# Optimization experiments

Hardware: AMD Instinct MI355X
Metric: run time of the kernel (lower is better)

The kernel has to match this reference:

```python
import jax, jax.numpy as jnp
import numpy as np

DIM = 1024
NUM_HEADS = 16
DIM_HEAD = 64
INNER = NUM_HEADS * DIM_HEAD  # 1024
SCALE = DIM_HEAD ** -0.5


def setup_inputs() -> dict:
    key = jax.random.key(0)
    ks = jax.random.split(key, 8)
    B, SQ, SK = 2, 2048, 4096
    x = jax.random.normal(ks[0], (B, SQ, DIM), dtype=jnp.float32)
    context = jax.random.normal(ks[1], (B, SK, DIM), dtype=jnp.float32)
    # LayerNorm params
    ln_gamma = jnp.ones((DIM,), jnp.float32)
    ln_beta = jnp.zeros((DIM,), jnp.float32)
    # Linear weights, stored as [in, out] so y = x @ W (torch Linear weight transposed)
    w_q = jax.random.normal(ks[2], (DIM, INNER), dtype=jnp.float32) / np.sqrt(DIM)
    w_kv = jax.random.normal(ks[3], (DIM, 2 * INNER), dtype=jnp.float32) / np.sqrt(DIM)
    w_out = jax.random.normal(ks[4], (INNER, DIM), dtype=jnp.float32) / np.sqrt(INNER)
    b_out = jnp.zeros((DIM,), jnp.float32)
    # torch init is 0.0 (tanh(0)=0); use a nonzero value so output/grads are nontrivial
    gate = jnp.array([0.5], jnp.float32)
    return {"x": x, "context": context, "ln_gamma": ln_gamma, "ln_beta": ln_beta,
            "w_q": w_q, "w_kv": w_kv, "w_out": w_out, "b_out": b_out, "gate": gate}


def _layernorm(x, gamma, beta, eps=1e-5):
    mu = jnp.mean(x, axis=-1, keepdims=True)
    var = jnp.mean(jnp.square(x - mu), axis=-1, keepdims=True)
    return (x - mu) * jax.lax.rsqrt(var + eps) * gamma + beta


def reference(x, context, ln_gamma, ln_beta, w_q, w_kv, w_out, b_out, gate):
    B, SQ, _ = x.shape
    SK = context.shape[1]
    xn = _layernorm(x, ln_gamma, ln_beta)
    q = (xn @ w_q).reshape(B, SQ, NUM_HEADS, DIM_HEAD)
    kv = context @ w_kv
    k, v = jnp.split(kv, 2, axis=-1)
    k = k.reshape(B, SK, NUM_HEADS, DIM_HEAD)
    v = v.reshape(B, SK, NUM_HEADS, DIM_HEAD)
    # scores: [B, H, SQ, SK]
    scores = jnp.einsum('bqhd,bkhd->bhqk', q * SCALE, k)
    attn = jax.nn.softmax(scores, axis=-1)
    out = jnp.einsum('bhqk,bkhd->bqhd', attn, v).reshape(B, SQ, INNER)
    out = out @ w_out + b_out
    return out * jnp.tanh(gate[0])
```

## Files before the change

### kernel.cpp

```cpp
#include <hip/hip_runtime.h>
#include <hip/hip_bf16.h>
#include <stdint.h>

#define DIMM  1024
#define NHEAD 16
#define DHEAD 64
#define BB    2
#define SQL   2048
#define SKL   4096
#define KVW   2048
#define NT    (SKL / 64)

typedef __attribute__((ext_vector_type(8))) short short8;
typedef __attribute__((ext_vector_type(4))) float f32x4;
typedef __attribute__((ext_vector_type(16))) float f32x16;
typedef __attribute__((ext_vector_type(4))) unsigned short us4;

typedef const __attribute__((address_space(1))) uint32_t gu32_t;
typedef __attribute__((address_space(3))) uint32_t lu32_t;

#define GLDS16(gp, lp) __builtin_amdgcn_global_load_lds((gu32_t*)(gp), (lu32_t*)(lp), 16, 0, 0)

static __device__ __forceinline__ unsigned short f2bf(float f) {
  union { float f; uint32_t u; } v; v.f = f;
  uint32_t r = v.u + 0x7fffu + ((v.u >> 16) & 1u);
  return (unsigned short)(r >> 16);
}

__global__ __launch_bounds__(256) void k_prep(const float* __restrict__ wq,
                                              const float* __restrict__ wkv,
                                              const float* __restrict__ wot,
                                              const float* __restrict__ x,
                                              const float* __restrict__ gamma,
                                              const float* __restrict__ beta,
                                              const float* __restrict__ ctx,
                                              unsigned short* __restrict__ WQT,
                                              unsigned short* __restrict__ WKVT,
                                              unsigned short* __restrict__ WOT,
                                              unsigned short* __restrict__ XN,
                                              unsigned short* __restrict__ CTXB) {
  const int bid = blockIdx.x;
  const int tid = threadIdx.x;

  if (bid < 4096) {
    __shared__ float tile[32][33];
    const float* in; unsigned short* out; int N, bx, by;
    if (bid < 1024)      {                    in = wq;  out = WQT;  N = 1024; bx = bid & 31; by = bid >> 5; }
    else if (bid < 3072) { int l = bid - 1024; in = wkv; out = WKVT; N = 2048; bx = l & 63; by = l >> 6; }
    else                 { int l = bid - 3072; in = wot; out = WOT;  N = 1024; bx = l & 31; by = l >> 5; }
    const int K = 1024;
    const int n0 = bx * 32, k0 = by * 32;
    const int tx = tid & 31, ty = tid >> 5;
    #pragma unroll
    for (int i = 0; i < 4; i++)
      tile[ty + i * 8][tx] = in[(size_t)(k0 + ty + i * 8) * N + n0 + tx];
    __syncthreads();
    #pragma unroll
    for (int i = 0; i < 4; i++)
      out[(size_t)(n0 + ty + i * 8) * K + k0 + tx] = f2bf(tile[tx][ty + i * 8]);
  } else if (bid < 8192) {
    const int row = bid - 4096;
    const float* xr = x + (size_t)row * DIMM;
    float4 v = *(const float4*)(xr + tid * 4);
    float s = v.x + v.y + v.z + v.w;
    float ss = v.x * v.x + v.y * v.y + v.z * v.z + v.w * v.w;
    #pragma unroll
    for (int m = 1; m < 64; m <<= 1) {
      s += __shfl_xor(s, m);
      ss += __shfl_xor(ss, m);
    }
    __shared__ float red[8];
    const int wid = tid >> 6, lane = tid & 63;
    if (lane == 0) { red[wid] = s; red[4 + wid] = ss; }
    __syncthreads();
    s = red[0] + red[1] + red[2] + red[3];
    ss = red[4] + red[5] + red[6] + red[7];
    float mu = s * (1.0f / DIMM);
    float var = ss * (1.0f / DIMM) - mu * mu;
    float rstd = rsqrtf(var + 1e-5f);
    float4 g = *(const float4*)(gamma + tid * 4);
    float4 bt = *(const float4*)(beta + tid * 4);
    us4 o;
    o.x = f2bf((v.x - mu) * rstd * g.x + bt.x);
    o.y = f2bf((v.y - mu) * rstd * g.y + bt.y);
    o.z = f2bf((v.z - mu) * rstd * g.z + bt.z);
    o.w = f2bf((v.w - mu) * rstd * g.w + bt.w);
    *(us4*)(XN + (size_t)row * DIMM + tid * 4) = o;
  } else {
    size_t i = ((size_t)(bid - 8192) * 256 + tid) * 8;
    float4 v0 = *(const float4*)(ctx + i);
    float4 v1 = *(const float4*)(ctx + i + 4);
    union { us4 h[2]; short8 s; } o;
    o.h[0].x = f2bf(v0.x); o.h[0].y = f2bf(v0.y); o.h[0].z = f2bf(v0.z); o.h[0].w = f2bf(v0.w);
    o.h[1].x = f2bf(v1.x); o.h[1].y = f2bf(v1.y); o.h[1].z = f2bf(v1.z); o.h[1].w = f2bf(v1.w);
    *(short8*)(CTXB + i) = o.s;
  }
}

__global__ __launch_bounds__(256) void k_proj(const unsigned short* __restrict__ CTXB,
                                              const unsigned short* __restrict__ XN,
                                              const unsigned short* __restrict__ WKVT,
                                              const unsigned short* __restrict__ WQT,
                                              unsigned short* __restrict__ KVB,
                                              unsigned short* __restrict__ QB) {
  __shared__ unsigned short lA[2][128 * 32];
  __shared__ unsigned short lB[2][128 * 32];
  const int tid = threadIdx.x;
  const int wid = tid >> 6, lane = tid & 63;
  const int kg = lane >> 4, lr = lane & 15;
  const int wr = wid >> 1, wc = wid & 1;
  const int K = 1024, nt = 32;

  const int bid = blockIdx.x;
  const int xcd = bid & 7;
  const int idx = bid >> 3;
  const bool isQ = (idx >= 128);
  int im, in_, N;
  const unsigned short* Ap;
  const unsigned short* Bw;
  unsigned short* Cout;
  if (isQ) { int q = idx - 128; im = xcd * 4 + (q & 3);   in_ = q >> 2;   Bw = WQT;  Cout = QB;  N = 1024; Ap = XN; }
  else     {                    im = xcd * 8 + (idx & 7); in_ = idx >> 3; Bw = WKVT; Cout = KVB; N = 2048; Ap = CTXB; }
  const size_t baseB = (size_t)in_ * 128 * K;
  const unsigned short* Abf = Ap + (size_t)im * 128 * K;

  int ed[2], grow[2], gcol[2];
  #pragma unroll
  for (int j = 0; j < 2; j++) {
    int e = wid * 1024 + j * 512 + lane * 8;
    ed[j] = e;
    int row = e >> 5;
    grow[j] = row;
    gcol[j] = (((e >> 3) & 3) ^ ((row >> 1) & 3)) << 3;
  }

  f32x4 acc[4][4];
  #pragma unroll
  for (int m = 0; m < 4; m++)
    #pragma unroll
    for (int n = 0; n < 4; n++) {
      f32x4 z = {0.0f, 0.0f, 0.0f, 0.0f};
      acc[m][n] = z;
    }

  auto STAGE = [&](int bufi, int t) {
    int k0 = t << 5;
    #pragma unroll
    for (int j = 0; j < 2; j++) {
      GLDS16(Abf + (size_t)grow[j] * K + k0 + gcol[j], &lA[bufi][ed[j]]);
      GLDS16(Bw + baseB + (size_t)grow[j] * K + k0 + gcol[j], &lB[bufi][ed[j]]);
    }
  };
  auto COMPUTE = [&](int bufi) {
    short8 a[4], b[4];
    #pragma unroll
    for (int m = 0; m < 4; m++) {
      int row = wr * 64 + m * 16 + lr;
      a[m] = *(const short8*)&lA[bufi][row * 32 + ((kg ^ ((row >> 1) & 3)) << 3)];
    }
    #pragma unroll
    for (int n = 0; n < 4; n++) {
      int row = wc * 64 + n * 16 + lr;
      b[n] = *(const short8*)&lB[bufi][row * 32 + ((kg ^ ((row >> 1) & 3)) << 3)];
    }
    #pragma unroll
    for (int m = 0; m < 4; m++)
      #pragma unroll
      for (int n = 0; n < 4; n++)
        acc[m][n] = __builtin_amdgcn_mfma_f32_16x16x32_bf16(a[m], b[n], acc[m][n], 0, 0, 0);
  };

  STAGE(0, 0);
  __syncthreads();
  int buf = 0;
  for (int t = 0; t < nt; t++) {
    if (t + 1 < nt) STAGE(buf ^ 1, t + 1);
    COMPUTE(buf);
    __syncthreads();
    buf ^= 1;
  }

  const int r0 = im * 128 + wr * 64;
  const int c0 = in_ * 128 + wc * 64;
  #pragma unroll
  for (int m = 0; m < 4; m++)
    #pragma unroll
    for (int n = 0; n < 4; n++)
      #pragma unroll
      for (int j = 0; j < 4; j++)
        Cout[(size_t)(r0 + m * 16 + kg * 4 + j) * N + c0 + n * 16 + lr] = f2bf(acc[m][n][j]);
}

__global__ __launch_bounds__(256) void k_out(const unsigned short* __restrict__ A,
                                             const unsigned short* __restrict__ BT,
                                             float* __restrict__ C,
                                             const float* __restrict__ bias,
                                             const float* __restrict__ gate) {
  __shared__ unsigned short lA[2][64 * 32];
  __shared__ unsigned short lB[2][128 * 32];
  const int tid = threadIdx.x;
  const int wid = tid >> 6, lane = tid & 63;
  const int kg = lane >> 4, lr = lane & 15;
  const int wr = wid >> 1, wc = wid & 1;
  const int K = 1024, nt = 32, N = 1024;

  const int bid = blockIdx.x;
  const int xcd = bid & 7;
  const int idx = bid >> 3;
  const int im = xcd * 8 + (idx & 7);
  const int in_ = idx >> 3;
  const size_t baseA = (size_t)im * 64 * K;
  const size_t baseB = (size_t)in_ * 128 * K;

  int eA, arow, acol;
  {
    int e = tid * 8;
    eA = e;
    int row = e >> 5;
    arow = row; acol = (((e >> 3) & 3) ^ ((row >> 1) & 3)) << 3;
  }
  int eB[2], brow[2], bcol[2];
  #pragma unroll
  for (int j = 0; j < 2; j++) {
    int e = tid * 8 + j * 2048;
    eB[j] = e;
    int row = e >> 5;
    brow[j] = row; bcol[j] = (((e >> 3) & 3) ^ ((row >> 1) & 3)) << 3;
  }

  f32x4 acc[2][4];
  #pragma unroll
  for (int m = 0; m < 2; m++)
    #pragma unroll
    for (int n = 0; n < 4; n++) {
      f32x4 z = {0.0f, 0.0f, 0.0f, 0.0f};
      acc[m][n] = z;
    }

  auto STAGE = [&](int bufi, int t) {
    int k0 = t << 5;
    GLDS16(A + baseA + (size_t)arow * K + k0 + acol, &lA[bufi][eA]);
    #pragma unroll
    for (int j = 0; j < 2; j++)
      GLDS16(BT + baseB + (size_t)brow[j] * K + k0 + bcol[j], &lB[bufi][eB[j]]);
  };

  STAGE(0, 0);
  __syncthreads();
  int buf = 0;
  for (int t = 0; t < nt; t++) {
    if (t + 1 < nt) STAGE(buf ^ 1, t + 1);
    short8 a[2], b[4];
    #pragma unroll
    for (int m = 0; m < 2; m++) {
      int row = wr * 32 + m * 16 + lr;
      a[m] = *(const short8*)&lA[buf][row * 32 + ((kg ^ ((row >> 1) & 3)) << 3)];
    }
    #pragma unroll
    for (int n = 0; n < 4; n++) {
      int row = wc * 64 + n * 16 + lr;
      b[n] = *(const short8*)&lB[buf][row * 32 + ((kg ^ ((row >> 1) & 3)) << 3)];
    }
    #pragma unroll
    for (int m = 0; m < 2; m++)
      #pragma unroll
      for (int n = 0; n < 4; n++)
        acc[m][n] = __builtin_amdgcn_mfma_f32_16x16x32_bf16(a[m], b[n], acc[m][n], 0, 0, 0);
    __syncthreads();
    buf ^= 1;
  }

  const int r0 = im * 64 + wr * 32;
  const int c0 = in_ * 128 + wc * 64;
  float gl = tanhf(gate[0]);
  #pragma unroll
  for (int m = 0; m < 2; m++)
    #pragma unroll
    for (int n = 0; n < 4; n++)
      #pragma unroll
      for (int j = 0; j < 4; j++) {
        int col = c0 + n * 16 + lr;
        C[(size_t)(r0 + m * 16 + kg * 4 + j) * N + col] = (acc[m][n][j] + bias[col]) * gl;
      }
}

__global__ __launch_bounds__(256, 4) void k_attn(const unsigned short* __restrict__ Q,
                                                 const unsigned short* __restrict__ KV,
                                                 unsigned short* __restrict__ O) {
  __shared__ unsigned short sK[2][64 * 64];
  __shared__ unsigned short sV[2][64 * 64];

  const int tid = threadIdx.x;
  const int wave = tid >> 6, lane = tid & 63;
  const int wq = wave & 1, wk = wave >> 1;
  const int l31 = lane & 31, hi = lane >> 5;

  const int wid_b = blockIdx.x;
  const int work = (wid_b & 7) * 128 + (wid_b >> 3);
  const int qb = work & 31, bh = work >> 5;
  const int b = bh >> 4, h = bh & 15;

  const unsigned short* Qp = Q + (size_t)b * SQL * DIMM + h * DHEAD;
  const unsigned short* Kp = KV + (size_t)b * SKL * KVW + h * DHEAD;
  const unsigned short* Vp = Kp + DIMM;

  const int qr0 = qb * 64 + wq * 32;

  const unsigned short* ksrc[2]; int kdst[2];
  const unsigned short* vsrc[2]; int vdst[2];
  #pragma unroll
  for (int j = 0; j < 2; j++) {
    int e = (tid + j * 256) * 8;
    int row = e >> 6;
    int col = (((e >> 3) & 7) ^ (row & 7)) << 3;
    ksrc[j] = Kp + (size_t)row * KVW + col;
    kdst[j] = e;
    int g = tid + j * 256;
    int key = (g >> 5) * 4 + ((g >> 1) & 3);
    int d0v = ((g >> 3) & 3) * 16 + (g & 1) * 8;
    vsrc[j] = Vp + (size_t)key * KVW + d0v;
    vdst[j] = g * 8;
  }

  auto STAGE = [&](int bufi, int kt) {
    size_t off = (size_t)kt * 64 * KVW;
    #pragma unroll
    for (int j = 0; j < 2; j++) GLDS16(ksrc[j] + off, &sK[bufi][kdst[j]]);
    #pragma unroll
    for (int j = 0; j < 2; j++) GLDS16(vsrc[j] + off, &sV[bufi][vdst[j]]);
  };

  short8 qa[4];
  #pragma unroll
  for (int t = 0; t < 4; t++) {
    short8 v = *(const short8*)(Qp + (size_t)(qr0 + l31) * DIMM + t * 16 + hi * 8);
    #pragma unroll
    for (int j = 0; j < 8; j++) {
      union { float f; uint32_t u; } c;
      c.u = ((uint32_t)(unsigned short)v[j]) << 16;
      v[j] = (short)f2bf(c.f * 0.1803368801111f);
    }
    qa[t] = v;
  }

  f32x16 oacc[2];
  #pragma unroll
  for (int d2 = 0; d2 < 2; d2++)
    #pragma unroll
    for (int r = 0; r < 16; r++) oacc[d2][r] = 0.0f;
  float rs = 0.0f;

  const uint32_t sVb0 = (uint32_t)(size_t)(lu32_t*)&sV[0][0] +
                        (uint32_t)(hi * 1024 + ((lane >> 4) & 1) * 128 + (lane & 15) * 8);

  STAGE(0, 0);
  __syncthreads();

  union u4s8 { uint32_t u[4]; short8 s; };

  int buf = 0;
  for (int kt = 0; kt < NT; kt++) {
    if (kt + 1 < NT) STAGE(buf ^ 1, kt + 1);

    short8 kbf[4];
    {
      int row = wk * 32 + l31;
      #pragma unroll
      for (int t = 0; t < 4; t++) {
        int gl = t * 2 + hi;
        kbf[t] = *(const short8*)&sK[buf][row * 64 + ((gl ^ (row & 7)) << 3)];
      }
    }

    f32x16 sc;
    #pragma unroll
    for (int r = 0; r < 16; r++) sc[r] = 0.0f;
    #pragma unroll
    for (int t = 0; t < 4; t++)
      sc = __builtin_amdgcn_mfma_f32_32x32x16_bf16(kbf[t], qa[t], sc, 0, 0, 0);

    float p[16];
    #pragma unroll
    for (int r = 0; r < 16; r++) {
      p[r] = __builtin_amdgcn_exp2f(sc[r]);
      rs += p[r];
    }
    uint32_t w[8];
    #pragma unroll
    for (int i = 0; i < 8; i++)
      asm("v_cvt_pk_bf16_f32 %0, %1, %2" : "=v"(w[i]) : "v"(p[2 * i]), "v"(p[2 * i + 1]));
    asm("v_permlane32_swap_b32 %0, %1" : "+v"(w[0]), "+v"(w[2]));
    asm("v_permlane32_swap_b32 %0, %1" : "+v"(w[1]), "+v"(w[3]));
    asm("v_permlane32_swap_b32 %0, %1" : "+v"(w[4]), "+v"(w[6]));
    asm("v_permlane32_swap_b32 %0, %1" : "+v"(w[5]), "+v"(w[7]));
    u4s8 paf[2];
    paf[0].u[0] = w[0]; paf[0].u[1] = w[1]; paf[0].u[2] = w[2]; paf[0].u[3] = w[3];
    paf[1].u[0] = w[4]; paf[1].u[1] = w[5]; paf[1].u[2] = w[6]; paf[1].u[3] = w[7];

    u4s8 vb[2][2];
    {
      uint32_t tb = sVb0 + (uint32_t)(buf * 8192 + wk * 4096);
      #pragma unroll
      for (int d2 = 0; d2 < 2; d2++)
        #pragma unroll
        for (int ks = 0; ks < 2; ks++) {
          uint2 t0, t1;
          uint32_t a0 = tb + (uint32_t)(ks * 2048 + d2 * 256);
          asm volatile("ds_read_b64_tr_b16 %0, %1" : "=v"(t0) : "v"(a0));
          asm volatile("ds_read_b64_tr_b16 %0, %1" : "=v"(t1) : "v"(a0 + 512u));
          vb[d2][ks].u[0] = t0.x; vb[d2][ks].u[1] = t0.y;
          vb[d2][ks].u[2] = t1.x; vb[d2][ks].u[3] = t1.y;
        }
    }
    asm volatile("s_waitcnt lgkmcnt(0)" ::: "memory");
    __builtin_amdgcn_sched_barrier(0);

    #pragma unroll
    for (int d2 = 0; d2 < 2; d2++)
      #pragma unroll
      for (int ks = 0; ks < 2; ks++)
        oacc[d2] = __builtin_amdgcn_mfma_f32_32x32x16_bf16(paf[ks].s, vb[d2][ks].s, oacc[d2], 0, 0, 0);

    __syncthreads();
    buf ^= 1;
  }

  float* sRed = (float*)&sK[0][0];
  float* sRs  = (float*)&sV[0][0];
  if (wk == 1) {
    #pragma unroll
    for (int d2 = 0; d2 < 2; d2++)
      #pragma unroll
      for (int r = 0; r < 16; r++)
        sRed[((wq * 2 + d2) * 16 + r) * 64 + lane] = oacc[d2][r];
    sRs[wq * 64 + lane] = rs;
  }
  __syncthreads();
  if (wk == 0) {
    #pragma unroll
    for (int d2 = 0; d2 < 2; d2++)
      #pragma unroll
      for (int r = 0; r < 16; r++)
        oacc[d2][r] += sRed[((wq * 2 + d2) * 16 + r) * 64 + lane];
    float rs2 = rs + sRs[wq * 64 + lane];
    float t = rs2 + __shfl_xor(rs2, 32);
    float inv = 1.0f / t;
    float rq[16];
    #pragma unroll
    for (int r = 0; r < 16; r++) {
      int rho = (r & 3) + 8 * (r >> 2) + 4 * hi;
      rq[r] = __shfl(inv, rho);
    }
    unsigned short* Op = O + (size_t)b * SQL * DIMM + h * DHEAD;
    #pragma unroll
    for (int d2 = 0; d2 < 2; d2++)
      #pragma unroll
      for (int r = 0; r < 16; r++) {
        int rho = (r & 3) + 8 * (r >> 2) + 4 * hi;
        Op[(size_t)(qr0 + rho) * DIMM + d2 * 32 + l31] = f2bf(oacc[d2][r] * rq[r]);
      }
  }
}

extern "C" void kernel_launch(void* const* d_in, const int* in_sizes, int n_in,
                              void* d_out, int out_size, void* d_ws, size_t ws_size,
                              hipStream_t stream) {
  (void)in_sizes; (void)n_in; (void)out_size; (void)ws_size;
  const float* x     = (const float*)d_in[0];
  const float* ctx   = (const float*)d_in[1];
  const float* gamma = (const float*)d_in[2];
  const float* beta  = (const float*)d_in[3];
  const float* w_q   = (const float*)d_in[4];
  const float* w_kv  = (const float*)d_in[5];
  const float* w_out = (const float*)d_in[6];
  const float* b_out = (const float*)d_in[7];
  const float* gate  = (const float*)d_in[8];
  float* out = (float*)d_out;
  char* ws = (char*)d_ws;

  unsigned short* XN   = (unsigned short*)(ws);
  unsigned short* QB   = (unsigned short*)(ws + (8ull  << 20));
  unsigned short* CTXB = (unsigned short*)(ws + (16ull << 20));
  unsigned short* KVB  = (unsigned short*)(ws + (32ull << 20));
  unsigned short* OB   = (unsigned short*)(ws + (64ull << 20));
  unsigned short* WQT  = (unsigned short*)(ws + (72ull << 20));
  unsigned short* WKVT = (unsigned short*)(ws + (74ull << 20));
  unsigned short* WOT  = (unsigned short*)(ws + (78ull << 20));

  k_prep<<<dim3(12288), dim3(256), 0, stream>>>(w_q, w_kv, w_out, x, gamma, beta, ctx,
                                                WQT, WKVT, WOT, XN, CTXB);
  k_proj<<<dim3(1280), dim3(256), 0, stream>>>(CTXB, XN, WKVT, WQT, KVB, QB);
  k_attn<<<dim3(1024), dim3(256), 0, stream>>>(QB, KVB, OB);
  k_out<<<dim3(512), dim3(256), 0, stream>>>(OB, WOT, out, b_out, gate);
}
```

Measured before the change: 200.9 us.

## Split attention key range across two blocks and add partial-sum reduction kernel

Each (batch, head, query-block) tile of the attention kernel is now split over two blocks, each covering half of the key tiles. The grid doubles to 2048 blocks. Each block writes an unnormalised bf16 partial output and its row sums into reused workspace. A new reduction kernel adds the two partials and divides by the combined row sum. This is meant to expose more parallelism and shorten the critical path per block. In exchange it adds an extra launch, roughly 16 MB of partial-output traffic, and bf16 rounding of the intermediate partials.

```diff
diff --git a/kernel.cpp b/kernel.cpp
--- a/kernel.cpp
+++ b/kernel.cpp
@@ -25,6 +25,9 @@
   union { float f; uint32_t u; } v; v.f = f;
   uint32_t r = v.u + 0x7fffu + ((v.u >> 16) & 1u);
   return (unsigned short)(r >> 16);
+}
+static __device__ __forceinline__ float bf2f(unsigned short h) {
+  union { float f; uint32_t u; } v; v.u = ((uint32_t)h) << 16; return v.f;
 }
 
 __global__ __launch_bounds__(256) void k_prep(const float* __restrict__ wq,
@@ -286,7 +289,8 @@
 
 __global__ __launch_bounds__(256, 4) void k_attn(const unsigned short* __restrict__ Q,
                                                  const unsigned short* __restrict__ KV,
-                                                 unsigned short* __restrict__ O) {
+                                                 unsigned short* __restrict__ OPART,
+                                                 float* __restrict__ RSPART) {
   __shared__ unsigned short sK[2][64 * 64];
   __shared__ unsigned short sV[2][64 * 64];
 
@@ -296,8 +300,10 @@
   const int l31 = lane & 31, hi = lane >> 5;
 
   const int wid_b = blockIdx.x;
-  const int work = (wid_b & 7) * 128 + (wid_b >> 3);
-  const int qb = work & 31, bh = work >> 5;
+  const int work = (wid_b & 7) * 256 + (wid_b >> 3);
+  const int half = work & 1;
+  const int w2 = work >> 1;
+  const int qb = w2 & 31, bh = w2 >> 5;
   const int b = bh >> 4, h = bh & 15;
 
   const unsigned short* Qp = Q + (size_t)b * SQL * DIMM + h * DHEAD;
@@ -305,6 +311,7 @@
   const unsigned short* Vp = Kp + DIMM;
 
   const int qr0 = qb * 64 + wq * 32;
+  const int kbeg = half * (NT / 2), kend = kbeg + NT / 2;
 
   const unsigned short* ksrc[2]; int kdst[2];
   const unsigned short* vsrc[2]; int vdst[2];
@@ -353,14 +360,14 @@
   const uint32_t sVb0 = (uint32_t)(size_t)(lu32_t*)&sV[0][0] +
                         (uint32_t)(hi * 1024 + ((lane >> 4) & 1) * 128 + (lane & 15) * 8);
 
-  STAGE(0, 0);
+  STAGE(0, kbeg);
   __syncthreads();
 
   union u4s8 { uint32_t u[4]; short8 s; };
 
   int buf = 0;
-  for (int kt = 0; kt < NT; kt++) {
-    if (kt + 1 < NT) STAGE(buf ^ 1, kt + 1);
+  for (int kt = kbeg; kt < kend; kt++) {
+    if (kt + 1 < kend) STAGE(buf ^ 1, kt + 1);
 
     short8 kbf[4];
     {
@@ -443,23 +450,51 @@
       for (int r = 0; r < 16; r++)
         oacc[d2][r] += sRed[((wq * 2 + d2) * 16 + r) * 64 + lane];
     float rs2 = rs + sRs[wq * 64 + lane];
-    float t = rs2 + __shfl_xor(rs2, 32);
-    float inv = 1.0f / t;
-    float rq[16];
-    #pragma unroll
-    for (int r = 0; r < 16; r++) {
-      int rho = (r & 3) + 8 * (r >> 2) + 4 * hi;
-      rq[r] = __shfl(inv, rho);
-    }
-    unsigned short* Op = O + (size_t)b * SQL * DIMM + h * DHEAD;
+    float tsum = rs2 + __shfl_xor(rs2, 32);
+
+    const size_t pb = ((size_t)(w2 * 2 + half)) * (64 * 64);
+    unsigned short* Pp = OPART + pb;
     #pragma unroll
     for (int d2 = 0; d2 < 2; d2++)
       #pragma unroll
       for (int r = 0; r < 16; r++) {
         int rho = (r & 3) + 8 * (r >> 2) + 4 * hi;
-        Op[(size_t)(qr0 + rho) * DIMM + d2 * 32 + l31] = f2bf(oacc[d2][r] * rq[r]);
+        Pp[(wq * 32 + rho) * 64 + d2 * 32 + l31] = f2bf(oacc[d2][r]);
       }
-  }
+    if (hi == 0)
+      RSPART[(size_t)(w2 * 2 + half) * 64 + wq * 32 + l31] = tsum;
+  }
+}
+
+__global__ __launch_bounds__(256) void k_red(const unsigned short* __restrict__ OPART,
+                                             const float* __restrict__ RSPART,
+                                             unsigned short* __restrict__ O) {
+  const int w2 = blockIdx.x;
+  const int qb = w2 & 31, bh = w2 >> 5;
+  const int b = bh >> 4, h = bh & 15;
+  const int tid = threadIdx.x;
+  const int rowl = tid >> 2;
+  const int c0 = (tid & 3) * 16;
+
+  const size_t p0 = ((size_t)(w2 * 2 + 0)) * 4096 + (size_t)rowl * 64 + c0;
+  const size_t p1 = ((size_t)(w2 * 2 + 1)) * 4096 + (size_t)rowl * 64 + c0;
+  float inv = 1.0f / (RSPART[(size_t)(w2 * 2 + 0) * 64 + rowl] +
+                      RSPART[(size_t)(w2 * 2 + 1) * 64 + rowl]);
+
+  short8 a0 = *(const short8*)&OPART[p0];
+  short8 a1 = *(const short8*)&OPART[p0 + 8];
+  short8 b0 = *(const short8*)&OPART[p1];
+  short8 b1 = *(const short8*)&OPART[p1 + 8];
+
+  short8 o0, o1;
+  #pragma unroll
+  for (int j = 0; j < 8; j++) {
+    o0[j] = (short)f2bf((bf2f((unsigned short)a0[j]) + bf2f((unsigned short)b0[j])) * inv);
+    o1[j] = (short)f2bf((bf2f((unsigned short)a1[j]) + bf2f((unsigned short)b1[j])) * inv);
+  }
+  unsigned short* Op = O + (size_t)b * SQL * DIMM + (size_t)(qb * 64 + rowl) * DIMM + h * DHEAD + c0;
+  *(short8*)Op = o0;
+  *(short8*)(Op + 8) = o1;
 }
 
 extern "C" void kernel_launch(void* const* d_in, const int* in_sizes, int n_in,
@@ -487,9 +522,13 @@
   unsigned short* WKVT = (unsigned short*)(ws + (74ull << 20));
   unsigned short* WOT  = (unsigned short*)(ws + (78ull << 20));
 
+  unsigned short* OPART = CTXB;
+  float*          RSPART = (float*)XN;
+
   k_prep<<<dim3(12288), dim3(256), 0, stream>>>(w_q, w_kv, w_out, x, gamma, beta, ctx,
                                                 WQT, WKVT, WOT, XN, CTXB);
   k_proj<<<dim3(1280), dim3(256), 0, stream>>>(CTXB, XN, WKVT, WQT, KVB, QB);
-  k_attn<<<dim3(1024), dim3(256), 0, stream>>>(QB, KVB, OB);
+  k_attn<<<dim3(2048), dim3(256), 0, stream>>>(QB, KVB, OPART, RSPART);
+  k_red<<<dim3(1024), dim3(256), 0, stream>>>(OPART, RSPART, OB);
   k_out<<<dim3(512), dim3(256), 0, stream>>>(OB, WOT, out, b_out, gate);
 }
```

New measurement: 205.8 us. +2.4%, slower.
